# Kernel optimization log

Hardware: AMD Instinct MI355X
Metric: run time of the kernel (lower is better)

Reference implementation:

```python
import jax, jax.numpy as jnp
import numpy as np

B, T, C, H = 1, 4096, 768, 12
D = C // H  # 64


def setup_inputs() -> dict:
    key = jax.random.key(0)
    ks = jax.random.split(key, 5)
    s = 0.02
    return {
        "x": jax.random.normal(ks[0], (B, T, C), dtype=jnp.float32),
        "Wk": jax.random.normal(ks[1], (C, C), dtype=jnp.float32) * s,
        "bk": jax.random.normal(ks[2], (C,), dtype=jnp.float32) * s,
        "Wq": jax.random.normal(ks[3], (C, C), dtype=jnp.float32) * s,
        "bq": jax.random.normal(ks[4], (C,), dtype=jnp.float32) * s,
    }


def reference(x, Wk, bk, Wq, bq):
    b, t, c = x.shape
    h, d = H, c // H
    # projections (value is raw x, as in the source module)
    k = (x @ Wk + bk).reshape(b, t, h, d).transpose(0, 2, 1, 3)  # [B,H,T,D]
    q = (x @ Wq + bq).reshape(b, t, h, d).transpose(0, 2, 1, 3)  # [B,H,T,D]
    v = x.reshape(b, t, h, d).transpose(0, 2, 1, 3)              # [B,H,T,D]
    # NOTE: source computes K @ Q^T (keys as rows), no 1/sqrt(d) scaling
    logits = jnp.einsum("bhid,bhjd->bhij", k, q)                 # [B,H,T,T]
    causal = jnp.tril(jnp.ones((t, t), dtype=bool))              # [T,T]
    masked = jnp.where(causal[None, None], logits, -jnp.inf)
    att = jax.nn.softmax(masked, axis=-1)
    y = jnp.einsum("bhij,bhjd->bhid", att, v)                    # [B,H,T,D]
    return y.transpose(0, 2, 1, 3).reshape(b, t, c)
```

## Files before the change

### kernel.cpp

```cpp
#include <hip/hip_runtime.h>
#include <hip/hip_bf16.h>
#include <math.h>

#define T_LEN 4096
#define C_DIM 768
#define H_NUM 12
#define D_DIM 64

typedef __bf16 bf16x8 __attribute__((ext_vector_type(8)));
typedef float f32x16 __attribute__((ext_vector_type(16)));

static __device__ __forceinline__ unsigned short bf16bits(float f) {
    return __builtin_bit_cast(unsigned short, __float2bfloat16(f));
}

template <typename TP>
static __device__ __forceinline__ void stp(TP* p, float v) {
    if constexpr (sizeof(TP) == 4) *p = v;
    else *p = __float2bfloat16(v);
}
template <typename TP>
static __device__ __forceinline__ float ldp(const TP* p) {
    if constexpr (sizeof(TP) == 4) return *p;
    else return __bfloat162float(*p);
}

__global__ __launch_bounds__(256) void prep_kernel(
    const float* __restrict__ x,
    const float* __restrict__ Wk, const float* __restrict__ Wq,
    __hip_bfloat16* __restrict__ Vt,
    __hip_bfloat16* __restrict__ xhi,
    __hip_bfloat16* __restrict__ xlo,
    __hip_bfloat16* __restrict__ wt) {
    __shared__ float tile[64][65];
    const int bx = blockIdx.x;
    const int tid = threadIdx.x;
    const int cl = tid & 63;
    const int rq = tid >> 6;
    if (bx < 768) {
        const int t0 = (bx & 63) * 64;
        const int c0 = (bx >> 6) * 64;
#pragma unroll
        for (int rr = 0; rr < 16; ++rr) {
            const int row = rr * 4 + rq;
            const float v = x[(size_t)(t0 + row) * C_DIM + c0 + cl];
            tile[row][cl] = v;
            const __hip_bfloat16 hb = __float2bfloat16(v);
            xhi[(size_t)(t0 + row) * C_DIM + c0 + cl] = hb;
            xlo[(size_t)(t0 + row) * C_DIM + c0 + cl] =
                __float2bfloat16(v - __bfloat162float(hb));
        }
        __syncthreads();
#pragma unroll
        for (int cc = 0; cc < 16; ++cc) {
            const int c = cc * 4 + rq;
            const int gc = c0 + c;
            const int h = gc >> 6, d = gc & 63;
            Vt[((size_t)h * D_DIM + d) * T_LEN + t0 + cl] =
                __float2bfloat16(tile[cl][c]);
        }
    } else {
        const int bz = bx - 768;
        const int w  = bz / 144;
        const int rem = bz - w * 144;
        const int k0 = (rem % 12) * 64;
        const int n0 = (rem / 12) * 64;
        const float* W = w ? Wq : Wk;
        __hip_bfloat16* o = wt + (size_t)w * C_DIM * C_DIM;
#pragma unroll
        for (int rr = 0; rr < 16; ++rr) {
            const int row = rr * 4 + rq;
            tile[row][cl] = W[(size_t)(k0 + row) * C_DIM + n0 + cl];
        }
        __syncthreads();
#pragma unroll
        for (int rr = 0; rr < 16; ++rr) {
            const int row = rr * 4 + rq;
            o[(size_t)(n0 + row) * C_DIM + k0 + cl] =
                __float2bfloat16(tile[cl][row]);
        }
    }
}

__global__ __launch_bounds__(256) void proj_mfma2(
    const __hip_bfloat16* __restrict__ xhi,
    const __hip_bfloat16* __restrict__ xlo,
    const __hip_bfloat16* __restrict__ wt,
    const float* __restrict__ bk, const float* __restrict__ bq,
    __hip_bfloat16* __restrict__ kout, __hip_bfloat16* __restrict__ qout) {

    __shared__ __align__(16) char AhiL[16384];
    __shared__ __align__(16) char AloL[16384];
    __shared__ __align__(16) char BL[8192];

    const int bid = blockIdx.x;
    const int wg  = (bid & 7) * 96 + (bid >> 3);
    const int mt  = wg / 24;
    const int nc  = wg - mt * 24;
    const int wsel = nc / 12;
    const int nt  = nc - wsel * 12;
    const int m0 = mt * 128, n0 = nt * 64;

    const int tid = threadIdx.x;
    const int wv = tid >> 6;
    const int lane = tid & 63;
    const int lm = lane & 31, hi = lane >> 5;

    const __hip_bfloat16* wb = wt + (size_t)wsel * C_DIM * C_DIM;

    f32x16 acc0 = {}, acc1 = {};
    const int arow = wv * 32 + lm;
    const int asw = arow & 7;
    const int bsw = lm & 7;

    for (int k0 = 0; k0 < C_DIM; k0 += 64) {
        __syncthreads();
#pragma unroll
        for (int it = 0; it < 4; ++it) {
            const int g = tid + it * 256;
            const int row = g >> 3, ch = g & 7;
            const int dst = row * 128 + ((ch ^ (row & 7)) << 4);
            *reinterpret_cast<uint4*>(AhiL + dst) =
                *reinterpret_cast<const uint4*>(
                    xhi + (size_t)(m0 + row) * C_DIM + k0 + ch * 8);
            *reinterpret_cast<uint4*>(AloL + dst) =
                *reinterpret_cast<const uint4*>(
                    xlo + (size_t)(m0 + row) * C_DIM + k0 + ch * 8);
        }
#pragma unroll
        for (int it = 0; it < 2; ++it) {
            const int g = tid + it * 256;
            const int row = g >> 3, ch = g & 7;
            const int dst = row * 128 + ((ch ^ (row & 7)) << 4);
            *reinterpret_cast<uint4*>(BL + dst) =
                *reinterpret_cast<const uint4*>(
                    wb + (size_t)(n0 + row) * C_DIM + k0 + ch * 8);
        }
        __syncthreads();

#pragma unroll
        for (int ki = 0; ki < 4; ++ki) {
            const int ch = ki * 2 + hi;
            const bf16x8 ah = *reinterpret_cast<const bf16x8*>(
                AhiL + arow * 128 + ((ch ^ asw) << 4));
            const bf16x8 al = *reinterpret_cast<const bf16x8*>(
                AloL + arow * 128 + ((ch ^ asw) << 4));
            const bf16x8 b0 = *reinterpret_cast<const bf16x8*>(
                BL + lm * 128 + ((ch ^ bsw) << 4));
            const bf16x8 b1 = *reinterpret_cast<const bf16x8*>(
                BL + (32 + lm) * 128 + ((ch ^ bsw) << 4));
            acc0 = __builtin_amdgcn_mfma_f32_32x32x16_bf16(ah, b0, acc0, 0, 0, 0);
            acc1 = __builtin_amdgcn_mfma_f32_32x32x16_bf16(ah, b1, acc1, 0, 0, 0);
            acc0 = __builtin_amdgcn_mfma_f32_32x32x16_bf16(al, b0, acc0, 0, 0, 0);
            acc1 = __builtin_amdgcn_mfma_f32_32x32x16_bf16(al, b1, acc1, 0, 0, 0);
        }
    }

    const float* bias = wsel ? bq : bk;
    __hip_bfloat16* out = wsel ? qout : kout;
    const int h = nt;
    const float bv0 = bias[n0 + lm];
    const float bv1 = bias[n0 + 32 + lm];
#pragma unroll
    for (int r = 0; r < 16; ++r) {
        const int cr = (r & 3) + 8 * (r >> 2) + 4 * hi;
        const int t = m0 + wv * 32 + cr;
        out[((size_t)h * T_LEN + t) * D_DIM + lm]      = __float2bfloat16(acc0[r] + bv0);
        out[((size_t)h * T_LEN + t) * D_DIM + 32 + lm] = __float2bfloat16(acc1[r] + bv1);
    }
}

__global__ __launch_bounds__(256) void vtx_only_kernel(
    const float* __restrict__ x, __hip_bfloat16* __restrict__ Vt) {
    __shared__ float tile[64][65];
    const int t0 = blockIdx.x * 64;
    const int c0 = blockIdx.y * 64;
    const int tid = threadIdx.x;
    const int cl = tid & 63;
    const int rq = tid >> 6;
#pragma unroll
    for (int rr = 0; rr < 16; ++rr) {
        const int row = rr * 4 + rq;
        tile[row][cl] = x[(size_t)(t0 + row) * C_DIM + c0 + cl];
    }
    __syncthreads();
#pragma unroll
    for (int cc = 0; cc < 16; ++cc) {
        const int c = cc * 4 + rq;
        const int gc = c0 + c;
        const int h = gc >> 6, d = gc & 63;
        Vt[((size_t)h * D_DIM + d) * T_LEN + t0 + cl] =
            __float2bfloat16(tile[cl][c]);
    }
}

__global__ __launch_bounds__(256) void proj_gemm(
    const float* __restrict__ x,
    const float* __restrict__ Wk, const float* __restrict__ bk,
    const float* __restrict__ Wq, const float* __restrict__ bq,
    __hip_bfloat16* __restrict__ kout, __hip_bfloat16* __restrict__ qout) {

    const float* W; const float* bias; __hip_bfloat16* out;
    if (blockIdx.z == 0) { W = Wk; bias = bk; out = kout; }
    else                 { W = Wq; bias = bq; out = qout; }

    __shared__ __align__(16) float As[32][68];
    __shared__ __align__(16) float Bs[32][68];

    const int tid = threadIdx.x;
    const int m0_blk = blockIdx.y * 64;
    const int n0_blk = blockIdx.x * 64;
    const int tx = tid & 15, ty = tid >> 4;
    const int mm = ty * 4, nn = tx * 4;
    float acc[4][4] = {};
    const int a_kq = tid & 7;
    const int a_m  = tid >> 3;
    const int b_n4 = (tid & 15) * 4;
    const int b_k  = tid >> 4;

    for (int k0 = 0; k0 < C_DIM; k0 += 32) {
#pragma unroll
        for (int half = 0; half < 2; ++half) {
            const int m = a_m + half * 32;
            const float4 av = *reinterpret_cast<const float4*>(
                &x[(size_t)(m0_blk + m) * C_DIM + k0 + a_kq * 4]);
            As[a_kq * 4 + 0][m] = av.x;
            As[a_kq * 4 + 1][m] = av.y;
            As[a_kq * 4 + 2][m] = av.z;
            As[a_kq * 4 + 3][m] = av.w;
        }
#pragma unroll
        for (int half = 0; half < 2; ++half) {
            const int kk = b_k + half * 16;
            *reinterpret_cast<float4*>(&Bs[kk][b_n4]) =
                *reinterpret_cast<const float4*>(
                    &W[(size_t)(k0 + kk) * C_DIM + n0_blk + b_n4]);
        }
        __syncthreads();
#pragma unroll
        for (int kk = 0; kk < 32; ++kk) {
            const float4 a4 = *reinterpret_cast<const float4*>(&As[kk][mm]);
            const float4 b4 = *reinterpret_cast<const float4*>(&Bs[kk][nn]);
            const float a_[4] = {a4.x, a4.y, a4.z, a4.w};
            const float b_[4] = {b4.x, b4.y, b4.z, b4.w};
#pragma unroll
            for (int i = 0; i < 4; ++i)
#pragma unroll
                for (int j = 0; j < 4; ++j)
                    acc[i][j] = fmaf(a_[i], b_[j], acc[i][j]);
        }
        __syncthreads();
    }

    const int h = blockIdx.x;
    const float4 bv = *reinterpret_cast<const float4*>(&bias[n0_blk + nn]);
    const float b_[4] = {bv.x, bv.y, bv.z, bv.w};
#pragma unroll
    for (int i = 0; i < 4; ++i) {
        const int t = m0_blk + mm + i;
        ushort4 o;
        o.x = bf16bits(acc[i][0] + b_[0]);
        o.y = bf16bits(acc[i][1] + b_[1]);
        o.z = bf16bits(acc[i][2] + b_[2]);
        o.w = bf16bits(acc[i][3] + b_[3]);
        *reinterpret_cast<ushort4*>(
            &out[((size_t)h * T_LEN + t) * D_DIM + nn]) = o;
    }
}

template <typename TP>
__global__ __launch_bounds__(256) void attn_split2(
    const __hip_bfloat16* __restrict__ K,
    const __hip_bfloat16* __restrict__ Q,
    const __hip_bfloat16* __restrict__ Vt,
    TP* __restrict__ pacc,
    float* __restrict__ pml) {

    __shared__ __align__(16) char QsB[2][8192];
    __shared__ __align__(16) char VsB[2][8192];

    const int bid = blockIdx.x;
    const int wg  = (bid & 7) * 120 + (bid >> 3);
    const int hh  = wg / 80;
    const int r   = 79 - (wg - hh * 80);
    int ib, s;
    if (r < 8)       { ib = r; s = 0; }
    else if (r < 24) { const int q = r - 8;  ib = 8 + (q >> 1);  s = q & 1; }
    else if (r < 48) { const int q = r - 24; ib = 16 + q / 3;    s = q - 3 * (q / 3); }
    else             { const int q = r - 48; ib = 24 + (q >> 2); s = q & 3; }

    const int tid  = threadIdx.x;
    const int wv   = tid >> 6;
    const int lane = tid & 63;
    const int lm   = lane & 31;
    const int hi   = lane >> 5;
    const int t    = ib * 4 + wv;
    const int iw   = t * 32;

    const int jt0  = s * 32;
    const int jend = min((s + 1) * 32, ib * 4 + 4);
    const int nsteps = (jend - jt0) >> 1;

    const __hip_bfloat16* kp = K + ((size_t)hh * T_LEN + iw + lm) * D_DIM + hi * 8;
    const bf16x8 bk0 = *reinterpret_cast<const bf16x8*>(kp + 0);
    const bf16x8 bk1 = *reinterpret_cast<const bf16x8*>(kp + 16);
    const bf16x8 bk2 = *reinterpret_cast<const bf16x8*>(kp + 32);
    const bf16x8 bk3 = *reinterpret_cast<const bf16x8*>(kp + 48);

    const __hip_bfloat16* qsc = Q  + ((size_t)hh * T_LEN + jt0 * 32) * D_DIM;
    const __hip_bfloat16* vsc = Vt + (size_t)hh * D_DIM * T_LEN + jt0 * 32;

    const int k0c = tid, k1c = tid + 256;
    const int lo0 = (k0c >> 3) * 128 + (((k0c & 7) ^ ((k0c >> 3) & 7)) << 4);
    const int lo1 = (k1c >> 3) * 128 + (((k1c & 7) ^ ((k1c >> 3) & 7)) << 4);
    const size_t vro0 = (size_t)(tid >> 3) * T_LEN + (tid & 7) * 8;
    const size_t vro1 = (size_t)((tid >> 3) + 32) * T_LEN + (tid & 7) * 8;

    uint4 rq0 = *reinterpret_cast<const uint4*>(qsc + (size_t)k0c * 8);
    uint4 rq1 = *reinterpret_cast<const uint4*>(qsc + (size_t)k1c * 8);
    uint4 rv0 = *reinterpret_cast<const uint4*>(vsc + vro0);
    uint4 rv1 = *reinterpret_cast<const uint4*>(vsc + vro1);
    *reinterpret_cast<uint4*>(QsB[0] + lo0) = rq0;
    *reinterpret_cast<uint4*>(QsB[0] + lo1) = rq1;
    *reinterpret_cast<uint4*>(VsB[0] + lo0) = rv0;
    *reinterpret_cast<uint4*>(VsB[0] + lo1) = rv1;
    __syncthreads();

    f32x16 acc0 = {}, acc1 = {};
    float m = -1e30f, lsum = 0.0f;

#define COMPUTE(SUB) do {                                                     \
    const int jt_ = jt0 + st * 2 + (SUB);                                     \
    if (jt_ <= t) {                                                           \
        const char* qb = QsB[cur];                                            \
        const char* vb = VsB[cur];                                            \
        const int qrow = (SUB) * 32 + lm;                                     \
        const int qsw = qrow & 7;                                             \
        const bf16x8 aq0 = *reinterpret_cast<const bf16x8*>(                  \
            qb + qrow * 128 + (((0 + hi) ^ qsw) << 4));                       \
        const bf16x8 aq1 = *reinterpret_cast<const bf16x8*>(                  \
            qb + qrow * 128 + (((2 + hi) ^ qsw) << 4));                       \
        const bf16x8 aq2 = *reinterpret_cast<const bf16x8*>(                  \
            qb + qrow * 128 + (((4 + hi) ^ qsw) << 4));                       \
        const bf16x8 aq3 = *reinterpret_cast<const bf16x8*>(                  \
            qb + qrow * 128 + (((6 + hi) ^ qsw) << 4));                       \
        f32x16 sc = {};                                                       \
        sc = __builtin_amdgcn_mfma_f32_32x32x16_bf16(aq0, bk0, sc, 0, 0, 0);  \
        sc = __builtin_amdgcn_mfma_f32_32x32x16_bf16(aq1, bk1, sc, 0, 0, 0);  \
        sc = __builtin_amdgcn_mfma_f32_32x32x16_bf16(aq2, bk2, sc, 0, 0, 0);  \
        sc = __builtin_amdgcn_mfma_f32_32x32x16_bf16(aq3, bk3, sc, 0, 0, 0);  \
        if (jt_ == t) {                                                       \
            _Pragma("unroll")                                                 \
            for (int rr = 0; rr < 16; ++rr) {                                 \
                const int jr = (rr & 3) + 8 * (rr >> 2) + 4 * hi;             \
                if (jr > lm) sc[rr] = -1e30f;                                 \
            }                                                                 \
        }                                                                     \
        float pmax = sc[0];                                                   \
        _Pragma("unroll")                                                     \
        for (int rr = 1; rr < 16; ++rr) pmax = fmaxf(pmax, sc[rr]);           \
        pmax = fmaxf(pmax, __shfl_xor(pmax, 32));                             \
        if (__any(pmax > m + 8.0f)) {                                         \
            const float mn = fmaxf(m, pmax);                                  \
            const float scl = __expf(m - mn);                                 \
            lsum *= scl;                                                      \
            _Pragma("unroll")                                                 \
            for (int rr = 0; rr < 16; ++rr) {                                 \
                const float sr = __shfl(scl, (rr & 3) + 8 * (rr >> 2) + 4 * hi); \
                acc0[rr] *= sr;                                               \
                acc1[rr] *= sr;                                               \
            }                                                                 \
            m = mn;                                                           \
        }                                                                     \
        float p[16];                                                          \
        _Pragma("unroll")                                                     \
        for (int rr = 0; rr < 16; ++rr) p[rr] = __expf(sc[rr] - m);           \
        float ls = 0.0f;                                                      \
        _Pragma("unroll")                                                     \
        for (int rr = 0; rr < 16; ++rr) ls += p[rr];                          \
        lsum += ls;                                                           \
        unsigned int w_[8];                                                   \
        _Pragma("unroll")                                                     \
        for (int kk = 0; kk < 8; ++kk)                                        \
            w_[kk] = (unsigned int)bf16bits(p[2 * kk]) |                      \
                     ((unsigned int)bf16bits(p[2 * kk + 1]) << 16);           \
        unsigned int pw_[8];                                                  \
        _Pragma("unroll")                                                     \
        for (int kk = 0; kk < 8; ++kk) pw_[kk] = __shfl_xor((int)w_[kk], 32); \
        const uint4 a0u = hi ? make_uint4(pw_[2], pw_[3], w_[2], w_[3])       \
                             : make_uint4(w_[0], w_[1], pw_[0], pw_[1]);      \
        const uint4 a1u = hi ? make_uint4(pw_[6], pw_[7], w_[6], w_[7])       \
                             : make_uint4(w_[4], w_[5], pw_[4], pw_[5]);      \
        const bf16x8 pa0 = __builtin_bit_cast(bf16x8, a0u);                   \
        const bf16x8 pa1 = __builtin_bit_cast(bf16x8, a1u);                   \
        const int d0 = lm, d1 = 32 + lm;                                      \
        const int vsw = lm & 7;                                               \
        const bf16x8 v00 = *reinterpret_cast<const bf16x8*>(                  \
            vb + d0 * 128 + ((((SUB) * 4 + 0 + hi) ^ vsw) << 4));             \
        const bf16x8 v01 = *reinterpret_cast<const bf16x8*>(                  \
            vb + d0 * 128 + ((((SUB) * 4 + 2 + hi) ^ vsw) << 4));             \
        const bf16x8 v10 = *reinterpret_cast<const bf16x8*>(                  \
            vb + d1 * 128 + ((((SUB) * 4 + 0 + hi) ^ vsw) << 4));             \
        const bf16x8 v11 = *reinterpret_cast<const bf16x8*>(                  \
            vb + d1 * 128 + ((((SUB) * 4 + 2 + hi) ^ vsw) << 4));             \
        acc0 = __builtin_amdgcn_mfma_f32_32x32x16_bf16(pa0, v00, acc0, 0,0,0);\
        acc0 = __builtin_amdgcn_mfma_f32_32x32x16_bf16(pa1, v01, acc0, 0,0,0);\
        acc1 = __builtin_amdgcn_mfma_f32_32x32x16_bf16(pa0, v10, acc1, 0,0,0);\
        acc1 = __builtin_amdgcn_mfma_f32_32x32x16_bf16(pa1, v11, acc1, 0,0,0);\
    }                                                                         \
} while (0)

    int cur = 0;
    for (int st = 0; st < nsteps; ++st) {
        const bool more = (st + 1 < nsteps);
        if (more) {
            rq0 = *reinterpret_cast<const uint4*>(qsc + (size_t)(st + 1) * 4096 + (size_t)k0c * 8);
            rq1 = *reinterpret_cast<const uint4*>(qsc + (size_t)(st + 1) * 4096 + (size_t)k1c * 8);
            rv0 = *reinterpret_cast<const uint4*>(vsc + vro0 + (size_t)(st + 1) * 64);
            rv1 = *reinterpret_cast<const uint4*>(vsc + vro1 + (size_t)(st + 1) * 64);
        }
        COMPUTE(0);
        COMPUTE(1);
        if (more) {
            char* qn = QsB[cur ^ 1];
            char* vn = VsB[cur ^ 1];
            *reinterpret_cast<uint4*>(qn + lo0) = rq0;
            *reinterpret_cast<uint4*>(qn + lo1) = rq1;
            *reinterpret_cast<uint4*>(vn + lo0) = rv0;
            *reinterpret_cast<uint4*>(vn + lo1) = rv1;
        }
        __syncthreads();
        cur ^= 1;
    }
#undef COMPUTE

    const int slot = (hh * 80 + r) * 4 + wv;
    const float lrow = lsum + __shfl_xor(lsum, 32);
    if (hi == 0) {
        pml[(size_t)slot * 64 + lm]      = m;
        pml[(size_t)slot * 64 + 32 + lm] = lrow;
    }
    TP* pa = pacc + (size_t)slot * 2048;
#pragma unroll
    for (int rr = 0; rr < 16; ++rr) {
        const int cr = (rr & 3) + 8 * (rr >> 2) + 4 * hi;
        stp(&pa[cr * 64 + lm],      acc0[rr]);
        stp(&pa[cr * 64 + 32 + lm], acc1[rr]);
    }
}

template <typename TP>
__global__ __launch_bounds__(256) void attn_merge(
    const TP* __restrict__ pacc, const float* __restrict__ pml,
    float* __restrict__ y) {
    const int b = blockIdx.x;
    const int h = b / 128;
    const int t = b - h * 128;
    const int ib = t >> 2, w = t & 3;
    const int ns = (t >> 5) + 1;
    int bb;
    if (ib < 8)       bb = ib;
    else if (ib < 16) bb = 8 + (ib - 8) * 2;
    else if (ib < 24) bb = 24 + (ib - 16) * 3;
    else              bb = 48 + (ib - 24) * 4;
    const int slot0 = (h * 80 + bb) * 4 + w;
    const int tid = threadIdx.x;
    const int row = tid >> 3;
    const int dq  = (tid & 7) * 8;

    float m0 = pml[(size_t)slot0 * 64 + row];
    float l0 = pml[(size_t)slot0 * 64 + 32 + row];
    float m1 = -1e30f, l1 = 0.f, m2 = -1e30f, l2 = 0.f, m3 = -1e30f, l3 = 0.f;
    if (ns > 1) { m1 = pml[(size_t)(slot0 + 4) * 64 + row];  l1 = pml[(size_t)(slot0 + 4) * 64 + 32 + row]; }
    if (ns > 2) { m2 = pml[(size_t)(slot0 + 8) * 64 + row];  l2 = pml[(size_t)(slot0 + 8) * 64 + 32 + row]; }
    if (ns > 3) { m3 = pml[(size_t)(slot0 + 12) * 64 + row]; l3 = pml[(size_t)(slot0 + 12) * 64 + 32 + row]; }
    const float M = fmaxf(fmaxf(m0, m1), fmaxf(m2, m3));
    const float w0 = __expf(m0 - M), w1 = __expf(m1 - M);
    const float w2 = __expf(m2 - M), w3 = __expf(m3 - M);
    const float L = l0 * w0 + l1 * w1 + l2 * w2 + l3 * w3;
    const float inv = 1.0f / L;

    float o[8] = {};
    {
        const TP* pa = pacc + (size_t)slot0 * 2048 + row * 64 + dq;
#pragma unroll
        for (int k = 0; k < 8; ++k) o[k] += ldp(&pa[k]) * w0;
    }
    if (ns > 1) {
        const TP* pa = pacc + (size_t)(slot0 + 4) * 2048 + row * 64 + dq;
#pragma unroll
        for (int k = 0; k < 8; ++k) o[k] += ldp(&pa[k]) * w1;
    }
    if (ns > 2) {
        const TP* pa = pacc + (size_t)(slot0 + 8) * 2048 + row * 64 + dq;
#pragma unroll
        for (int k = 0; k < 8; ++k) o[k] += ldp(&pa[k]) * w2;
    }
    if (ns > 3) {
        const TP* pa = pacc + (size_t)(slot0 + 12) * 2048 + row * 64 + dq;
#pragma unroll
        for (int k = 0; k < 8; ++k) o[k] += ldp(&pa[k]) * w3;
    }
    float* yp = &y[(size_t)(t * 32 + row) * C_DIM + h * D_DIM + dq];
    float4 o0, o1;
    o0.x = o[0] * inv; o0.y = o[1] * inv; o0.z = o[2] * inv; o0.w = o[3] * inv;
    o1.x = o[4] * inv; o1.y = o[5] * inv; o1.z = o[6] * inv; o1.w = o[7] * inv;
    *reinterpret_cast<float4*>(yp + 0) = o0;
    *reinterpret_cast<float4*>(yp + 4) = o1;
}

__global__ __launch_bounds__(256) void attn_flat(
    const __hip_bfloat16* __restrict__ K,
    const __hip_bfloat16* __restrict__ Q,
    const __hip_bfloat16* __restrict__ Vt,
    float* __restrict__ y) {

    const int u  = blockIdx.x * 4 + (threadIdx.x >> 6);
    const int h  = u % H_NUM;
    const int itile = (T_LEN / 32 - 1) - u / H_NUM;
    const int iw = itile * 32;
    const int lane = threadIdx.x & 63;
    const int lm = lane & 31;
    const int hi = lane >> 5;

    const __hip_bfloat16* kp = K + ((size_t)h * T_LEN + iw + lm) * D_DIM + hi * 8;
    const bf16x8 bk0 = *reinterpret_cast<const bf16x8*>(kp + 0);
    const bf16x8 bk1 = *reinterpret_cast<const bf16x8*>(kp + 16);
    const bf16x8 bk2 = *reinterpret_cast<const bf16x8*>(kp + 32);
    const bf16x8 bk3 = *reinterpret_cast<const bf16x8*>(kp + 48);

    f32x16 acc0 = {}, acc1 = {};
    float m = -1e30f, lsum = 0.0f;

    const __hip_bfloat16* qrow  = Q  + ((size_t)h * T_LEN + lm) * D_DIM + hi * 8;
    const __hip_bfloat16* vrow0 = Vt + ((size_t)h * D_DIM + lm) * T_LEN + hi * 8;
    const __hip_bfloat16* vrow1 = vrow0 + (size_t)32 * T_LEN;

    for (int j0 = 0; j0 <= iw; j0 += 32) {
        const __hip_bfloat16* qp = qrow + (size_t)j0 * D_DIM;
        const bf16x8 aq0 = *reinterpret_cast<const bf16x8*>(qp + 0);
        const bf16x8 aq1 = *reinterpret_cast<const bf16x8*>(qp + 16);
        const bf16x8 aq2 = *reinterpret_cast<const bf16x8*>(qp + 32);
        const bf16x8 aq3 = *reinterpret_cast<const bf16x8*>(qp + 48);

        f32x16 sc = {};
        sc = __builtin_amdgcn_mfma_f32_32x32x16_bf16(aq0, bk0, sc, 0, 0, 0);
        sc = __builtin_amdgcn_mfma_f32_32x32x16_bf16(aq1, bk1, sc, 0, 0, 0);
        sc = __builtin_amdgcn_mfma_f32_32x32x16_bf16(aq2, bk2, sc, 0, 0, 0);
        sc = __builtin_amdgcn_mfma_f32_32x32x16_bf16(aq3, bk3, sc, 0, 0, 0);

        if (j0 == iw) {
#pragma unroll
            for (int r = 0; r < 16; ++r) {
                const int jr = (r & 3) + 8 * (r >> 2) + 4 * hi;
                if (jr > lm) sc[r] = -1e30f;
            }
        }

        float pmax = sc[0];
#pragma unroll
        for (int r = 1; r < 16; ++r) pmax = fmaxf(pmax, sc[r]);
        pmax = fmaxf(pmax, __shfl_xor(pmax, 32));

        if (__any(pmax > m + 8.0f)) {
            const float mn = fmaxf(m, pmax);
            const float scl = __expf(m - mn);
            lsum *= scl;
#pragma unroll
            for (int r = 0; r < 16; ++r) {
                const float sr = __shfl(scl, (r & 3) + 8 * (r >> 2) + 4 * hi);
                acc0[r] *= sr;
                acc1[r] *= sr;
            }
            m = mn;
        }

        float p[16];
#pragma unroll
        for (int r = 0; r < 16; ++r) p[r] = __expf(sc[r] - m);
        float ls = 0.0f;
#pragma unroll
        for (int r = 0; r < 16; ++r) ls += p[r];
        lsum += ls;

        unsigned int w[8];
#pragma unroll
        for (int k = 0; k < 8; ++k)
            w[k] = (unsigned int)bf16bits(p[2 * k]) |
                   ((unsigned int)bf16bits(p[2 * k + 1]) << 16);
        unsigned int pw[8];
#pragma unroll
        for (int k = 0; k < 8; ++k) pw[k] = __shfl_xor((int)w[k], 32);

        const uint4 a0u = hi ? make_uint4(pw[2], pw[3], w[2], w[3])
                             : make_uint4(w[0], w[1], pw[0], pw[1]);
        const uint4 a1u = hi ? make_uint4(pw[6], pw[7], w[6], w[7])
                             : make_uint4(w[4], w[5], pw[4], pw[5]);
        const bf16x8 pa0 = __builtin_bit_cast(bf16x8, a0u);
        const bf16x8 pa1 = __builtin_bit_cast(bf16x8, a1u);

        const bf16x8 v00 = *reinterpret_cast<const bf16x8*>(vrow0 + j0);
        const bf16x8 v01 = *reinterpret_cast<const bf16x8*>(vrow0 + j0 + 16);
        const bf16x8 v10 = *reinterpret_cast<const bf16x8*>(vrow1 + j0);
        const bf16x8 v11 = *reinterpret_cast<const bf16x8*>(vrow1 + j0 + 16);

        acc0 = __builtin_amdgcn_mfma_f32_32x32x16_bf16(pa0, v00, acc0, 0, 0, 0);
        acc0 = __builtin_amdgcn_mfma_f32_32x32x16_bf16(pa1, v01, acc0, 0, 0, 0);
        acc1 = __builtin_amdgcn_mfma_f32_32x32x16_bf16(pa0, v10, acc1, 0, 0, 0);
        acc1 = __builtin_amdgcn_mfma_f32_32x32x16_bf16(pa1, v11, acc1, 0, 0, 0);
    }

    const float lt = lsum + __shfl_xor(lsum, 32);
    const float linv = 1.0f / lt;
#pragma unroll
    for (int r = 0; r < 16; ++r) {
        const int cr = (r & 3) + 8 * (r >> 2) + 4 * hi;
        const int row = iw + cr;
        const float li = __shfl(linv, cr);
        y[(size_t)row * C_DIM + h * D_DIM + lm]      = acc0[r] * li;
        y[(size_t)row * C_DIM + h * D_DIM + 32 + lm] = acc1[r] * li;
    }
}

extern "C" void kernel_launch(void* const* d_in, const int* in_sizes, int n_in,
                              void* d_out, int out_size, void* d_ws, size_t ws_size,
                              hipStream_t stream) {
    const float* x  = (const float*)d_in[0];
    const float* Wk = (const float*)d_in[1];
    const float* bk = (const float*)d_in[2];
    const float* Wq = (const float*)d_in[3];
    const float* bq = (const float*)d_in[4];
    float* out = (float*)d_out;

    const size_t np = (size_t)T_LEN * C_DIM;
    const size_t NSLOT = 3840;
    __hip_bfloat16* kbuf  = (__hip_bfloat16*)d_ws;
    __hip_bfloat16* qbuf  = kbuf + np;
    __hip_bfloat16* vtbuf = qbuf + np;
    char* after_kqv = (char*)(vtbuf + np);
    __hip_bfloat16* wtbuf = (__hip_bfloat16*)after_kqv;

    const size_t wt_bytes   = 2 * (size_t)C_DIM * C_DIM * sizeof(__hip_bfloat16);
    const size_t pacc_f32_b = NSLOT * 2048 * sizeof(float);
    const size_t pacc_b16_b = NSLOT * 2048 * sizeof(__hip_bfloat16);
    const size_t pml_b      = NSLOT * 64 * sizeof(float);
    const size_t base_b     = 3 * np * sizeof(__hip_bfloat16);
    const size_t needC = base_b + wt_bytes;
    const size_t needB = base_b + pacc_b16_b + pml_b;
    const size_t needA = base_b + pacc_f32_b + pml_b;

    __hip_bfloat16* xhi = (__hip_bfloat16*)d_out;
    __hip_bfloat16* xlo = xhi + np;

    if (ws_size >= needC) {
        prep_kernel<<<1056, 256, 0, stream>>>(x, Wk, Wq, vtbuf, xhi, xlo, wtbuf);
        proj_mfma2<<<768, 256, 0, stream>>>(xhi, xlo, wtbuf, bk, bq, kbuf, qbuf);
    } else {
        dim3 gv(T_LEN / 64, C_DIM / 64);
        vtx_only_kernel<<<gv, 256, 0, stream>>>(x, vtbuf);
        dim3 g1(C_DIM / 64, T_LEN / 64, 2);
        proj_gemm<<<g1, 256, 0, stream>>>(x, Wk, bk, Wq, bq, kbuf, qbuf);
    }

    if (ws_size >= needA) {
        float* pacc = (float*)after_kqv;
        float* pml  = (float*)(after_kqv + pacc_f32_b);
        attn_split2<float><<<960, 256, 0, stream>>>(kbuf, qbuf, vtbuf, pacc, pml);
        attn_merge<float><<<1536, 256, 0, stream>>>(pacc, pml, out);
    } else if (ws_size >= needB) {
        __hip_bfloat16* pacc = (__hip_bfloat16*)after_kqv;
        float* pml = (float*)(after_kqv + pacc_b16_b);
        attn_split2<__hip_bfloat16><<<960, 256, 0, stream>>>(kbuf, qbuf, vtbuf, pacc, pml);
        attn_merge<__hip_bfloat16><<<1536, 256, 0, stream>>>(pacc, pml, out);
    } else {
        attn_flat<<<384, 256, 0, stream>>>(kbuf, qbuf, vtbuf, out);
    }
}
```

Measured before the change: 184.0 us.

## Halve attention split segment length and fold log2e into K for exp2

Templates the split-KV attention kernel on segment length and switches the default path from 32-tile to 16-tile segments. This gives 1728 work groups instead of 960, for better load balance across CUs, and makes the merge kernel combine up to 8 partials generically. K is pre-scaled by log2(e) in the projection so softmax can use exp2f instead of __expf. The cost is more partial-result traffic and workspace, and a larger merge reduction.

```diff
diff --git a/kernel.cpp b/kernel.cpp
--- a/kernel.cpp
+++ b/kernel.cpp
@@ -9,6 +9,8 @@
 
 typedef __bf16 bf16x8 __attribute__((ext_vector_type(8)));
 typedef float f32x16 __attribute__((ext_vector_type(16)));
+
+#define LOG2E 1.4426950408889634f
 
 static __device__ __forceinline__ unsigned short bf16bits(float f) {
     return __builtin_bit_cast(unsigned short, __float2bfloat16(f));
@@ -158,6 +160,7 @@
 
     const float* bias = wsel ? bq : bk;
     __hip_bfloat16* out = wsel ? qout : kout;
+    const float kscale = wsel ? 1.0f : LOG2E;
     const int h = nt;
     const float bv0 = bias[n0 + lm];
     const float bv1 = bias[n0 + 32 + lm];
@@ -165,8 +168,8 @@
     for (int r = 0; r < 16; ++r) {
         const int cr = (r & 3) + 8 * (r >> 2) + 4 * hi;
         const int t = m0 + wv * 32 + cr;
-        out[((size_t)h * T_LEN + t) * D_DIM + lm]      = __float2bfloat16(acc0[r] + bv0);
-        out[((size_t)h * T_LEN + t) * D_DIM + 32 + lm] = __float2bfloat16(acc1[r] + bv1);
+        out[((size_t)h * T_LEN + t) * D_DIM + lm]      = __float2bfloat16((acc0[r] + bv0) * kscale);
+        out[((size_t)h * T_LEN + t) * D_DIM + 32 + lm] = __float2bfloat16((acc1[r] + bv1) * kscale);
     }
 }
 
@@ -201,8 +204,9 @@
     __hip_bfloat16* __restrict__ kout, __hip_bfloat16* __restrict__ qout) {
 
     const float* W; const float* bias; __hip_bfloat16* out;
-    if (blockIdx.z == 0) { W = Wk; bias = bk; out = kout; }
-    else                 { W = Wq; bias = bq; out = qout; }
+    float sc;
+    if (blockIdx.z == 0) { W = Wk; bias = bk; out = kout; sc = LOG2E; }
+    else                 { W = Wq; bias = bq; out = qout; sc = 1.0f; }
 
     __shared__ __align__(16) float As[32][68];
     __shared__ __align__(16) float Bs[32][68];
@@ -259,16 +263,16 @@
     for (int i = 0; i < 4; ++i) {
         const int t = m0_blk + mm + i;
         ushort4 o;
-        o.x = bf16bits(acc[i][0] + b_[0]);
-        o.y = bf16bits(acc[i][1] + b_[1]);
-        o.z = bf16bits(acc[i][2] + b_[2]);
-        o.w = bf16bits(acc[i][3] + b_[3]);
+        o.x = bf16bits((acc[i][0] + b_[0]) * sc);
+        o.y = bf16bits((acc[i][1] + b_[1]) * sc);
+        o.z = bf16bits((acc[i][2] + b_[2]) * sc);
+        o.w = bf16bits((acc[i][3] + b_[3]) * sc);
         *reinterpret_cast<ushort4*>(
             &out[((size_t)h * T_LEN + t) * D_DIM + nn]) = o;
     }
 }
 
-template <typename TP>
+template <typename TP, int SEGT>
 __global__ __launch_bounds__(256) void attn_split2(
     const __hip_bfloat16* __restrict__ K,
     const __hip_bfloat16* __restrict__ Q,
@@ -276,18 +280,27 @@
     TP* __restrict__ pacc,
     float* __restrict__ pml) {
 
+    constexpr int GDIV = SEGT / 4;
+    constexpr int NGRP = 32 / GDIV;
+    constexpr int PER_HEAD = GDIV * NGRP * (NGRP + 1) / 2;
+    constexpr int CHUNK = (12 * PER_HEAD) / 8;
+
     __shared__ __align__(16) char QsB[2][8192];
     __shared__ __align__(16) char VsB[2][8192];
 
     const int bid = blockIdx.x;
-    const int wg  = (bid & 7) * 120 + (bid >> 3);
-    const int hh  = wg / 80;
-    const int r   = 79 - (wg - hh * 80);
-    int ib, s;
-    if (r < 8)       { ib = r; s = 0; }
-    else if (r < 24) { const int q = r - 8;  ib = 8 + (q >> 1);  s = q & 1; }
-    else if (r < 48) { const int q = r - 24; ib = 16 + q / 3;    s = q - 3 * (q / 3); }
-    else             { const int q = r - 48; ib = 24 + (q >> 2); s = q & 3; }
+    const int wg  = (bid & 7) * CHUNK + (bid >> 3);
+    const int hh  = wg / PER_HEAD;
+    const int r   = PER_HEAD - 1 - (wg - hh * PER_HEAD);
+    int g = 0, base = 0;
+    for (;;) {
+        const int cnt = GDIV * (g + 1);
+        if (r < base + cnt) break;
+        base += cnt; ++g;
+    }
+    const int rem = r - base;
+    const int ib  = g * GDIV + rem / (g + 1);
+    const int s   = rem - (rem / (g + 1)) * (g + 1);
 
     const int tid  = threadIdx.x;
     const int wv   = tid >> 6;
@@ -297,8 +310,8 @@
     const int t    = ib * 4 + wv;
     const int iw   = t * 32;
 
-    const int jt0  = s * 32;
-    const int jend = min((s + 1) * 32, ib * 4 + 4);
+    const int jt0  = s * SEGT;
+    const int jend = min((s + 1) * SEGT, ib * 4 + 4);
     const int nsteps = (jend - jt0) >> 1;
 
     const __hip_bfloat16* kp = K + ((size_t)hh * T_LEN + iw + lm) * D_DIM + hi * 8;
@@ -362,7 +375,7 @@
         pmax = fmaxf(pmax, __shfl_xor(pmax, 32));                             \
         if (__any(pmax > m + 8.0f)) {                                         \
             const float mn = fmaxf(m, pmax);                                  \
-            const float scl = __expf(m - mn);                                 \
+            const float scl = exp2f(m - mn);                                  \
             lsum *= scl;                                                      \
             _Pragma("unroll")                                                 \
             for (int rr = 0; rr < 16; ++rr) {                                 \
@@ -374,7 +387,7 @@
         }                                                                     \
         float p[16];                                                          \
         _Pragma("unroll")                                                     \
-        for (int rr = 0; rr < 16; ++rr) p[rr] = __expf(sc[rr] - m);           \
+        for (int rr = 0; rr < 16; ++rr) p[rr] = exp2f(sc[rr] - m);            \
         float ls = 0.0f;                                                      \
         _Pragma("unroll")                                                     \
         for (int rr = 0; rr < 16; ++rr) ls += p[rr];                          \
@@ -434,7 +447,7 @@
     }
 #undef COMPUTE
 
-    const int slot = (hh * 80 + r) * 4 + wv;
+    const int slot = (hh * PER_HEAD + r) * 4 + wv;
     const float lrow = lsum + __shfl_xor(lsum, 32);
     if (hi == 0) {
         pml[(size_t)slot * 64 + lm]      = m;
@@ -449,57 +462,51 @@
     }
 }
 
-template <typename TP>
+template <typename TP, int SEGT>
 __global__ __launch_bounds__(256) void attn_merge(
     const TP* __restrict__ pacc, const float* __restrict__ pml,
     float* __restrict__ y) {
+    constexpr int GDIV = SEGT / 4;
+    constexpr int NGRP = 32 / GDIV;
+    constexpr int PER_HEAD = GDIV * NGRP * (NGRP + 1) / 2;
+
     const int b = blockIdx.x;
     const int h = b / 128;
     const int t = b - h * 128;
     const int ib = t >> 2, w = t & 3;
-    const int ns = (t >> 5) + 1;
-    int bb;
-    if (ib < 8)       bb = ib;
-    else if (ib < 16) bb = 8 + (ib - 8) * 2;
-    else if (ib < 24) bb = 24 + (ib - 16) * 3;
-    else              bb = 48 + (ib - 24) * 4;
-    const int slot0 = (h * 80 + bb) * 4 + w;
+    const int g = ib / GDIV;
+    const int ns = g + 1;
+    const int bb = GDIV * g * (g + 1) / 2 + (ib % GDIV) * (g + 1);
+    const int slot0 = (h * PER_HEAD + bb) * 4 + w;
     const int tid = threadIdx.x;
     const int row = tid >> 3;
     const int dq  = (tid & 7) * 8;
 
-    float m0 = pml[(size_t)slot0 * 64 + row];
-    float l0 = pml[(size_t)slot0 * 64 + 32 + row];
-    float m1 = -1e30f, l1 = 0.f, m2 = -1e30f, l2 = 0.f, m3 = -1e30f, l3 = 0.f;
-    if (ns > 1) { m1 = pml[(size_t)(slot0 + 4) * 64 + row];  l1 = pml[(size_t)(slot0 + 4) * 64 + 32 + row]; }
-    if (ns > 2) { m2 = pml[(size_t)(slot0 + 8) * 64 + row];  l2 = pml[(size_t)(slot0 + 8) * 64 + 32 + row]; }
-    if (ns > 3) { m3 = pml[(size_t)(slot0 + 12) * 64 + row]; l3 = pml[(size_t)(slot0 + 12) * 64 + 32 + row]; }
-    const float M = fmaxf(fmaxf(m0, m1), fmaxf(m2, m3));
-    const float w0 = __expf(m0 - M), w1 = __expf(m1 - M);
-    const float w2 = __expf(m2 - M), w3 = __expf(m3 - M);
-    const float L = l0 * w0 + l1 * w1 + l2 * w2 + l3 * w3;
+    float ms[NGRP], ls[NGRP];
+#pragma unroll
+    for (int si = 0; si < NGRP; ++si) {
+        if (si < ns) {
+            ms[si] = pml[(size_t)(slot0 + 4 * si) * 64 + row];
+            ls[si] = pml[(size_t)(slot0 + 4 * si) * 64 + 32 + row];
+        } else { ms[si] = -1e30f; ls[si] = 0.0f; }
+    }
+    float M = ms[0];
+#pragma unroll
+    for (int si = 1; si < NGRP; ++si) M = fmaxf(M, ms[si]);
+    float wt_[NGRP];
+    float L = 0.0f;
+#pragma unroll
+    for (int si = 0; si < NGRP; ++si) { wt_[si] = exp2f(ms[si] - M); L += ls[si] * wt_[si]; }
     const float inv = 1.0f / L;
 
     float o[8] = {};
-    {
-        const TP* pa = pacc + (size_t)slot0 * 2048 + row * 64 + dq;
-#pragma unroll
-        for (int k = 0; k < 8; ++k) o[k] += ldp(&pa[k]) * w0;
-    }
-    if (ns > 1) {
-        const TP* pa = pacc + (size_t)(slot0 + 4) * 2048 + row * 64 + dq;
-#pragma unroll
-        for (int k = 0; k < 8; ++k) o[k] += ldp(&pa[k]) * w1;
-    }
-    if (ns > 2) {
-        const TP* pa = pacc + (size_t)(slot0 + 8) * 2048 + row * 64 + dq;
-#pragma unroll
-        for (int k = 0; k < 8; ++k) o[k] += ldp(&pa[k]) * w2;
-    }
-    if (ns > 3) {
-        const TP* pa = pacc + (size_t)(slot0 + 12) * 2048 + row * 64 + dq;
-#pragma unroll
-        for (int k = 0; k < 8; ++k) o[k] += ldp(&pa[k]) * w3;
+#pragma unroll
+    for (int si = 0; si < NGRP; ++si) {
+        if (si < ns) {
+            const TP* pa = pacc + (size_t)(slot0 + 4 * si) * 2048 + row * 64 + dq;
+#pragma unroll
+            for (int k = 0; k < 8; ++k) o[k] += ldp(&pa[k]) * wt_[si];
+        }
     }
     float* yp = &y[(size_t)(t * 32 + row) * C_DIM + h * D_DIM + dq];
     float4 o0, o1;
@@ -564,7 +571,7 @@
 
         if (__any(pmax > m + 8.0f)) {
             const float mn = fmaxf(m, pmax);
-            const float scl = __expf(m - mn);
+            const float scl = exp2f(m - mn);
             lsum *= scl;
 #pragma unroll
             for (int r = 0; r < 16; ++r) {
@@ -577,7 +584,7 @@
 
         float p[16];
 #pragma unroll
-        for (int r = 0; r < 16; ++r) p[r] = __expf(sc[r] - m);
+        for (int r = 0; r < 16; ++r) p[r] = exp2f(sc[r] - m);
         float ls = 0.0f;
 #pragma unroll
         for (int r = 0; r < 16; ++r) ls += p[r];
@@ -633,21 +640,20 @@
     float* out = (float*)d_out;
 
     const size_t np = (size_t)T_LEN * C_DIM;
-    const size_t NSLOT = 3840;
+    const size_t NSLOT_F = 12 * 144 * 4;
+    const size_t NSLOT_C = 12 * 80 * 4;
     __hip_bfloat16* kbuf  = (__hip_bfloat16*)d_ws;
     __hip_bfloat16* qbuf  = kbuf + np;
     __hip_bfloat16* vtbuf = qbuf + np;
     char* after_kqv = (char*)(vtbuf + np);
     __hip_bfloat16* wtbuf = (__hip_bfloat16*)after_kqv;
 
-    const size_t wt_bytes   = 2 * (size_t)C_DIM * C_DIM * sizeof(__hip_bfloat16);
-    const size_t pacc_f32_b = NSLOT * 2048 * sizeof(float);
-    const size_t pacc_b16_b = NSLOT * 2048 * sizeof(__hip_bfloat16);
-    const size_t pml_b      = NSLOT * 64 * sizeof(float);
-    const size_t base_b     = 3 * np * sizeof(__hip_bfloat16);
-    const size_t needC = base_b + wt_bytes;
-    const size_t needB = base_b + pacc_b16_b + pml_b;
-    const size_t needA = base_b + pacc_f32_b + pml_b;
+    const size_t wt_bytes  = 2 * (size_t)C_DIM * C_DIM * sizeof(__hip_bfloat16);
+    const size_t base_b    = 3 * np * sizeof(__hip_bfloat16);
+    const size_t needC     = base_b + wt_bytes;
+    const size_t needFineA = base_b + NSLOT_F * 2048 * 4 + NSLOT_F * 64 * 4;
+    const size_t needFineB = base_b + NSLOT_F * 2048 * 2 + NSLOT_F * 64 * 4;
+    const size_t needCoarB = base_b + NSLOT_C * 2048 * 2 + NSLOT_C * 64 * 4;
 
     __hip_bfloat16* xhi = (__hip_bfloat16*)d_out;
     __hip_bfloat16* xlo = xhi + np;
@@ -662,16 +668,21 @@
         proj_gemm<<<g1, 256, 0, stream>>>(x, Wk, bk, Wq, bq, kbuf, qbuf);
     }
 
-    if (ws_size >= needA) {
+    if (ws_size >= needFineA) {
         float* pacc = (float*)after_kqv;
-        float* pml  = (float*)(after_kqv + pacc_f32_b);
-        attn_split2<float><<<960, 256, 0, stream>>>(kbuf, qbuf, vtbuf, pacc, pml);
-        attn_merge<float><<<1536, 256, 0, stream>>>(pacc, pml, out);
-    } else if (ws_size >= needB) {
+        float* pml  = (float*)(after_kqv + NSLOT_F * 2048 * 4);
+        attn_split2<float, 16><<<1728, 256, 0, stream>>>(kbuf, qbuf, vtbuf, pacc, pml);
+        attn_merge<float, 16><<<1536, 256, 0, stream>>>(pacc, pml, out);
+    } else if (ws_size >= needFineB) {
         __hip_bfloat16* pacc = (__hip_bfloat16*)after_kqv;
-        float* pml = (float*)(after_kqv + pacc_b16_b);
-        attn_split2<__hip_bfloat16><<<960, 256, 0, stream>>>(kbuf, qbuf, vtbuf, pacc, pml);
-        attn_merge<__hip_bfloat16><<<1536, 256, 0, stream>>>(pacc, pml, out);
+        float* pml = (float*)(after_kqv + NSLOT_F * 2048 * 2);
+        attn_split2<__hip_bfloat16, 16><<<1728, 256, 0, stream>>>(kbuf, qbuf, vtbuf, pacc, pml);
+        attn_merge<__hip_bfloat16, 16><<<1536, 256, 0, stream>>>(pacc, pml, out);
+    } else if (ws_size >= needCoarB) {
+        __hip_bfloat16* pacc = (__hip_bfloat16*)after_kqv;
+        float* pml = (float*)(after_kqv + NSLOT_C * 2048 * 2);
+        attn_split2<__hip_bfloat16, 32><<<960, 256, 0, stream>>>(kbuf, qbuf, vtbuf, pacc, pml);
+        attn_merge<__hip_bfloat16, 32><<<1536, 256, 0, stream>>>(pacc, pml, out);
     } else {
         attn_flat<<<384, 256, 0, stream>>>(kbuf, qbuf, vtbuf, out);
     }
```

Measured after the change: 192.2 us. +4.5%, slower.
